# Kernel optimization log

Measured on AMD Instinct MI355X. Metric: run time of the kernel, lower is better.

## Reference

```python
import jax, jax.numpy as jnp
import numpy as np

EMB, HEADS = 1024, 16
HEAD_DIM = EMB // HEADS


def _linear(x, W, b):
    # torch nn.Linear convention: x @ W.T + b, W: [out, in]
    return jnp.einsum('bse,oe->bso', x, W) + b


def setup_inputs() -> dict:
    key = jax.random.key(0)
    ks = jax.random.split(key, 11)
    B, S = 2, 2048
    sc = 1.0 / np.sqrt(EMB)
    inp = {
        'x': jax.random.normal(ks[0], (B, S, EMB), dtype=jnp.float32),
        'y': jax.random.normal(ks[1], (B, S, EMB), dtype=jnp.float32),
        'mask': jnp.ones((B, S, S), dtype=jnp.int32),
        'Wq': jax.random.normal(ks[2], (EMB, EMB), dtype=jnp.float32) * sc,
        'bq': jax.random.normal(ks[3], (EMB,), dtype=jnp.float32) * sc,
        'Wk': jax.random.normal(ks[4], (EMB, EMB), dtype=jnp.float32) * sc,
        'bk': jax.random.normal(ks[5], (EMB,), dtype=jnp.float32) * sc,
        'Wv': jax.random.normal(ks[6], (EMB, EMB), dtype=jnp.float32) * sc,
        'bv': jax.random.normal(ks[7], (EMB,), dtype=jnp.float32) * sc,
        'Wo': jax.random.normal(ks[8], (EMB, EMB), dtype=jnp.float32) * sc,
        'bo': jax.random.normal(ks[9], (EMB,), dtype=jnp.float32) * sc,
    }
    return inp


def reference(x, y, mask, Wq, bq, Wk, bk, Wv, bv, Wo, bo):
    B, S, _ = x.shape
    q = _linear(x, Wq, bq).reshape(B, S, HEADS, HEAD_DIM).transpose(0, 2, 1, 3)
    k = _linear(y, Wk, bk).reshape(B, -1, HEADS, HEAD_DIM).transpose(0, 2, 1, 3)
    v = _linear(y, Wv, bv).reshape(B, -1, HEADS, HEAD_DIM).transpose(0, 2, 1, 3)
    # scores: [B, H, Sq, Sk]
    score = jnp.einsum('bhqd,bhkd->bhqk', q, k) / jnp.sqrt(jnp.float32(HEAD_DIM))
    # NOTE: original torch code calls score.masked_fill(...) without assignment,
    # so the mask has no effect on the computation (faithfully ignored here).
    weights = jax.nn.softmax(score, axis=-1)
    attn = jnp.einsum('bhqk,bhkd->bhqd', weights, v)
    attn = attn.transpose(0, 2, 1, 3).reshape(B, S, EMB)
    # dropout is identity in eval mode
    return _linear(attn, Wo, bo)
```

## Files before the change

kernel.cpp:

```cpp
#include <hip/hip_runtime.h>
#include <cstdint>
#include <cstddef>

#define BB 2
#define SS 2048
#define EE 1024
#define HH 16
#define DD 64

typedef __attribute__((ext_vector_type(8))) short short8;
typedef __attribute__((ext_vector_type(4))) short shortx4;
typedef __attribute__((ext_vector_type(8))) unsigned short ushort8;
typedef __attribute__((ext_vector_type(4))) unsigned short ush4;
typedef __attribute__((ext_vector_type(4))) float floatx4;

#define MFMA32(a, b, c) __builtin_amdgcn_mfma_f32_16x16x32_bf16((a), (b), (c), 0, 0, 0)
#define MFMA16(a, b, c) __builtin_amdgcn_mfma_f32_16x16x16bf16_1k((a), (b), (c), 0, 0, 0)

#define QSCALE 0.18033688011112042f

#define G2L16(g, l)                                                        \
    __builtin_amdgcn_global_load_lds(                                      \
        (const __attribute__((address_space(1))) void*)(g),                \
        (__attribute__((address_space(3))) void*)(l), 16, 0, 0)

__device__ __forceinline__ unsigned short f2bf(float f) {
    unsigned int u = __float_as_uint(f);
    u += 0x7fffu + ((u >> 16) & 1u);
    return (unsigned short)(u >> 16);
}

__device__ __forceinline__ unsigned int pkbf(float a, float b) {
    return __builtin_amdgcn_perm(__float_as_uint(b) + 0x8000u,
                                 __float_as_uint(a) + 0x8000u, 0x07060302u);
}

__global__ __launch_bounds__(256) void k_cvt(
    const float* __restrict__ x, unsigned short* __restrict__ xb,
    const float* __restrict__ y, unsigned short* __restrict__ yb,
    const float* __restrict__ w0, unsigned short* __restrict__ d0,
    const float* __restrict__ w1, unsigned short* __restrict__ d1,
    const float* __restrict__ w2, unsigned short* __restrict__ d2,
    const float* __restrict__ w3, unsigned short* __restrict__ d3)
{
    const int g = blockIdx.y;
    if (g >= 2 && blockIdx.x >= 256) return;
    const float* s = (g == 0) ? x : (g == 1) ? y : (g == 2) ? w0
                   : (g == 3) ? w1 : (g == 4) ? w2 : w3;
    unsigned short* d = (g == 0) ? xb : (g == 1) ? yb : (g == 2) ? d0
                      : (g == 3) ? d1 : (g == 4) ? d2 : d3;
    const size_t i = ((size_t)blockIdx.x * 256 + threadIdx.x) * 16;
    floatx4 f0 = *(const floatx4*)(s + i);
    floatx4 f1 = *(const floatx4*)(s + i + 4);
    floatx4 f2 = *(const floatx4*)(s + i + 8);
    floatx4 f3 = *(const floatx4*)(s + i + 12);
    ushort8 o0, o1;
#pragma unroll
    for (int j = 0; j < 4; ++j) { o0[j] = f2bf(f0[j]); o0[j + 4] = f2bf(f1[j]); }
#pragma unroll
    for (int j = 0; j < 4; ++j) { o1[j] = f2bf(f2[j]); o1[j + 4] = f2bf(f3[j]); }
    *(ushort8*)(d + i) = o0;
    *(ushort8*)(d + i + 8) = o1;
}

template <int MT, int OMODE>
__device__ __forceinline__ void gemm_body(
    const unsigned short* __restrict__ A, const unsigned short* __restrict__ W,
    const float* __restrict__ bias, void* __restrict__ Cv, float oscale,
    int m0, int n0,
    unsigned short* As0, unsigned short* As1, unsigned short* As2,
    unsigned short* Bs0, unsigned short* Bs1, unsigned short* Bs2)
{
    constexpr int K = 1024, N = 1024, LDT = 32;
    constexpr int MFR = MT / 32;
    constexpr int KEEP = (MT == 128) ? 8 : 6;
    const int t = threadIdx.x;
    const int lane = t & 63, w = t >> 6;
    const int q = lane >> 4, c = lane & 15;
    const int wm = w & 1, wn = w >> 1;
    const int lr = lane >> 2, lc = (lane & 3) * 8;

    const unsigned short* gA0 = A + (size_t)(m0 + w * (MT / 4) + lr) * K + lc;
    const unsigned short* gA1 = gA0 + 16 * K;
    const unsigned short* gB0 = W + (size_t)(n0 + w * 32 + lr) * K + lc;
    const unsigned short* gB1 = gB0 + 16 * K;
    unsigned short* lA0 = As0 + (w * (MT / 4)) * LDT;
    unsigned short* lA1 = As1 + (w * (MT / 4)) * LDT;
    unsigned short* lA2 = As2 + (w * (MT / 4)) * LDT;
    unsigned short* lB0 = Bs0 + (w * 32) * LDT;
    unsigned short* lB1 = Bs1 + (w * 32) * LDT;
    unsigned short* lB2 = Bs2 + (w * 32) * LDT;

    floatx4 acc[MFR][4] = {};

    auto compute = [&](const unsigned short* Ah, const unsigned short* Bh) {
        short8 af[MFR], bfr[4];
#pragma unroll
        for (int mi = 0; mi < MFR; ++mi)
            af[mi] = *(const short8*)
                &Ah[(wm * (MFR * 16) + mi * 16 + c) * LDT + q * 8];
#pragma unroll
        for (int ni = 0; ni < 4; ++ni)
            bfr[ni] = *(const short8*)
                &Bh[(wn * 64 + ni * 16 + c) * LDT + q * 8];
#pragma unroll
        for (int mi = 0; mi < MFR; ++mi)
#pragma unroll
            for (int ni = 0; ni < 4; ++ni)
                acc[mi][ni] = MFMA32(af[mi], bfr[ni], acc[mi][ni]);
    };

    auto stage = [&](int nk, unsigned short* lA, unsigned short* lB) {
        G2L16(gA0 + nk, lA);
        if constexpr (MT == 128) G2L16(gA1 + nk, lA + 16 * LDT);
        G2L16(gB0 + nk, lB);
        G2L16(gB1 + nk, lB + 16 * LDT);
    };

    auto phase = [&](int knext, unsigned short* lAn, unsigned short* lBn,
                     const unsigned short* Ac, const unsigned short* Bc) {
        __builtin_amdgcn_s_barrier();
        stage(knext & (K - 1), lAn, lBn);
        asm volatile("s_waitcnt vmcnt(%0)" :: "n"(KEEP) : "memory");
        __builtin_amdgcn_s_barrier();
        __builtin_amdgcn_sched_barrier(0);
        compute(Ac, Bc);
    };

    stage(0, lA0, lB0);
    stage(32, lA1, lB1);

    for (int g = 0; g < 10; ++g) {
        const int kb = g * 96;
        phase(kb +  64, lA2, lB2, As0, Bs0);
        phase(kb +  96, lA0, lB0, As1, Bs1);
        phase(kb + 128, lA1, lB1, As2, Bs2);
    }
    phase(1056, lA2, lB2, As0, Bs0);
    phase(1088, lA0, lB0, As1, Bs1);
    asm volatile("s_waitcnt vmcnt(0)" ::: "memory");

#pragma unroll
    for (int ni = 0; ni < 4; ++ni) {
        const int col = n0 + wn * 64 + ni * 16 + c;
        const float bv = bias[col];
#pragma unroll
        for (int mi = 0; mi < MFR; ++mi)
#pragma unroll
            for (int r = 0; r < 4; ++r) {
                const int row = m0 + wm * (MFR * 16) + mi * 16 + q * 4 + r;
                const float v = (acc[mi][ni][r] + bv) * oscale;
                if constexpr (OMODE == 0) {
                    ((unsigned short*)Cv)[(size_t)row * N + col] = f2bf(v);
                } else if constexpr (OMODE == 1) {
                    const int b = row >> 11, s = row & 2047;
                    ((unsigned short*)Cv)[((size_t)(b * 1024 + col)) * SS + s] = f2bf(v);
                } else {
                    ((float*)Cv)[(size_t)row * N + col] = v;
                }
            }
    }
}

__global__ __launch_bounds__(256) void k_gemm_qkv(
    const unsigned short* __restrict__ x, const unsigned short* __restrict__ y,
    const unsigned short* __restrict__ Wq, const float* __restrict__ bq,
    const unsigned short* __restrict__ Wk, const float* __restrict__ bk,
    const unsigned short* __restrict__ Wv, const float* __restrict__ bv,
    unsigned short* __restrict__ Q, unsigned short* __restrict__ Ko,
    unsigned short* __restrict__ Vt)
{
    __shared__ __align__(16) unsigned short As0[128 * 32], As1[128 * 32],
                                            As2[128 * 32];
    __shared__ __align__(16) unsigned short Bs0[128 * 32], Bs1[128 * 32],
                                            Bs2[128 * 32];
    const int m0 = blockIdx.y * 128;
    const int nt = blockIdx.x;
    const int g = nt >> 3;
    const int n0 = (nt & 7) * 128;
    if (g == 0) {
        gemm_body<128, 0>(x, Wq, bq, Q, QSCALE, m0, n0,
                          As0, As1, As2, Bs0, Bs1, Bs2);
    } else if (g == 1) {
        gemm_body<128, 0>(y, Wk, bk, Ko, 1.0f, m0, n0,
                          As0, As1, As2, Bs0, Bs1, Bs2);
    } else {
        gemm_body<128, 1>(y, Wv, bv, Vt, 1.0f, m0, n0,
                          As0, As1, As2, Bs0, Bs1, Bs2);
    }
}

__global__ __launch_bounds__(256) void k_gemm_out(
    const unsigned short* __restrict__ A, const unsigned short* __restrict__ W,
    const float* __restrict__ bias, float* __restrict__ C)
{
    __shared__ __align__(16) unsigned short As0[64 * 32], As1[64 * 32],
                                            As2[64 * 32];
    __shared__ __align__(16) unsigned short Bs0[128 * 32], Bs1[128 * 32],
                                            Bs2[128 * 32];
    gemm_body<64, 2>(A, W, bias, C, 1.0f, blockIdx.y * 64, blockIdx.x * 128,
                     As0, As1, As2, Bs0, Bs1, Bs2);
}

__global__ __launch_bounds__(512, 4) void k_attn(
    const unsigned short* __restrict__ Q, const unsigned short* __restrict__ K,
    const unsigned short* __restrict__ Vt, unsigned short* __restrict__ O)
{
    constexpr int LDK = 72;
    constexpr int TSZ = 64 * LDK + 64 * 64;
    __shared__ __align__(16) unsigned short smem[2 * 2 * TSZ];
    float* Ob = (float*)smem;

    const int bh = blockIdx.x, qt = blockIdx.y;
    const int b = bh >> 4, h = bh & 15;
    const int t = threadIdx.x, w = t >> 6;
    const int ws = w >> 2;
    const int wq = w & 3;
    const int lane = t & 63, q = lane >> 4, c = lane & 15;

    unsigned short* Sb = smem + ws * (2 * TSZ);

    short8 qb[2][2];
#pragma unroll
    for (int g = 0; g < 2; ++g) {
        const size_t qoff =
            (size_t)(b * SS + qt * 128 + wq * 32 + g * 16 + c) * EE + h * DD + q * 8;
        qb[g][0] = *(const short8*)(Q + qoff);
        qb[g][1] = *(const short8*)(Q + qoff + 32);
    }

    floatx4 o[2][4] = {};
    floatx4 lacc[2] = {};
    const shortx4 ones = {(short)0x3F80, (short)0x3F80, (short)0x3F80, (short)0x3F80};

    const int ts = t & 255;
    const int sr = ts >> 2, sp = (ts & 3) * 16;
    const int vkey = (sr & 15) << 2;
    const unsigned short* Kg =
        K + (size_t)(b * SS + ws * 1024 + sr) * EE + h * DD + sp;
    const unsigned short* Vg =
        Vt + ((size_t)bh * DD + sr) * SS + ws * 1024 + sp;

    {
        const ushort8* gk = (const ushort8*)Kg;
        ushort8 k0 = gk[0], k1 = gk[1];
        const ushort8* gv = (const ushort8*)Vg;
        ushort8 v0 = gv[0], v1 = gv[1];
        unsigned short* Ks = Sb;
        unsigned short* Vs = Sb + 64 * LDK;
        *(ushort8*)&Ks[sr * LDK + sp] = k0;
        *(ushort8*)&Ks[sr * LDK + sp + 8] = k1;
        *(ush4*)&Vs[sr * 64 + ((sp +  0) ^ vkey)] =
            __builtin_shufflevector(v0, v0, 0, 1, 2, 3);
        *(ush4*)&Vs[sr * 64 + ((sp +  4) ^ vkey)] =
            __builtin_shufflevector(v0, v0, 4, 5, 6, 7);
        *(ush4*)&Vs[sr * 64 + ((sp +  8) ^ vkey)] =
            __builtin_shufflevector(v1, v1, 0, 1, 2, 3);
        *(ush4*)&Vs[sr * 64 + ((sp + 12) ^ vkey)] =
            __builtin_shufflevector(v1, v1, 4, 5, 6, 7);
    }

#pragma unroll 2
    for (int it = 0; it < 16; ++it) {
        const unsigned short* Ks = Sb + (it & 1) * TSZ;
        const unsigned short* Vs = Ks + 64 * LDK;
        __syncthreads();

        const int nit = (it + 1) & 15;
        ushort8 pk0, pk1, pv0, pv1;
        {
            const ushort8* gk = (const ushort8*)(Kg + (size_t)nit * 64 * EE);
            pk0 = gk[0]; pk1 = gk[1];
            const ushort8* gv = (const ushort8*)(Vg + nit * 64);
            pv0 = gv[0]; pv1 = gv[1];
        }

#pragma unroll
        for (int tt = 0; tt < 4; ++tt) {
            const short8 ka0 = *(const short8*)&Ks[(tt * 16 + c) * LDK + q * 8];
            const short8 ka1 = *(const short8*)&Ks[(tt * 16 + c) * LDK + 32 + q * 8];
            shortx4 pa[2];
#pragma unroll
            for (int g = 0; g < 2; ++g) {
                floatx4 s = {0.f, 0.f, 0.f, 0.f};
                s = MFMA32(ka0, qb[g][0], s);
                s = MFMA32(ka1, qb[g][1], s);
                union { unsigned int u[2]; shortx4 v; } pk;
                pk.u[0] = pkbf(__builtin_amdgcn_exp2f(s[0]),
                               __builtin_amdgcn_exp2f(s[1]));
                pk.u[1] = pkbf(__builtin_amdgcn_exp2f(s[2]),
                               __builtin_amdgcn_exp2f(s[3]));
                pa[g] = pk.v;
            }
#pragma unroll
            for (int nd = 0; nd < 4; ++nd) {
                const shortx4 vb = *(const shortx4*)
                    &Vs[(nd * 16 + c) * 64 + (((tt * 4 + q) ^ c) << 2)];
                o[0][nd] = MFMA16(pa[0], vb, o[0][nd]);
                o[1][nd] = MFMA16(pa[1], vb, o[1][nd]);
            }
            lacc[0] = MFMA16(pa[0], ones, lacc[0]);
            lacc[1] = MFMA16(pa[1], ones, lacc[1]);
        }

        {
            unsigned short* Kn = Sb + ((it + 1) & 1) * TSZ;
            unsigned short* Vn = Kn + 64 * LDK;
            *(ushort8*)&Kn[sr * LDK + sp] = pk0;
            *(ushort8*)&Kn[sr * LDK + sp + 8] = pk1;
            *(ush4*)&Vn[sr * 64 + ((sp +  0) ^ vkey)] =
                __builtin_shufflevector(pv0, pv0, 0, 1, 2, 3);
            *(ush4*)&Vn[sr * 64 + ((sp +  4) ^ vkey)] =
                __builtin_shufflevector(pv0, pv0, 4, 5, 6, 7);
            *(ush4*)&Vn[sr * 64 + ((sp +  8) ^ vkey)] =
                __builtin_shufflevector(pv1, pv1, 0, 1, 2, 3);
            *(ush4*)&Vn[sr * 64 + ((sp + 12) ^ vkey)] =
                __builtin_shufflevector(pv1, pv1, 4, 5, 6, 7);
        }
    }

    __syncthreads();
    if (ws == 1) {
#pragma unroll
        for (int g = 0; g < 2; ++g) {
#pragma unroll
            for (int nd = 0; nd < 4; ++nd)
#pragma unroll
                for (int r = 0; r < 4; ++r)
                    Ob[(wq * 32 + g * 16 + q * 4 + r) * 66 + nd * 16 + c] =
                        o[g][nd][r];
            if (c == 0) {
#pragma unroll
                for (int r = 0; r < 4; ++r)
                    Ob[(wq * 32 + g * 16 + q * 4 + r) * 66 + 64] = lacc[g][r];
            }
        }
    }
    __syncthreads();
    if (ws == 0) {
#pragma unroll
        for (int g = 0; g < 2; ++g) {
            float linv[4];
#pragma unroll
            for (int r = 0; r < 4; ++r) {
                const int rr = wq * 32 + g * 16 + q * 4 + r;
#pragma unroll
                for (int nd = 0; nd < 4; ++nd)
                    o[g][nd][r] += Ob[rr * 66 + nd * 16 + c];
                linv[r] = __builtin_amdgcn_rcpf(lacc[g][r] + Ob[rr * 66 + 64]);
            }
            const int orow = b * SS + qt * 128 + wq * 32 + g * 16;
#pragma unroll
            for (int nd = 0; nd < 4; ++nd)
#pragma unroll
                for (int r = 0; r < 4; ++r)
                    O[(size_t)(orow + q * 4 + r) * EE + h * DD + nd * 16 + c] =
                        f2bf(o[g][nd][r] * linv[r]);
        }
    }
}

extern "C" void kernel_launch(void* const* d_in, const int* in_sizes, int n_in,
                              void* d_out, int out_size, void* d_ws, size_t ws_size,
                              hipStream_t stream)
{
    const float* x  = (const float*)d_in[0];
    const float* y  = (const float*)d_in[1];
    const float* Wq = (const float*)d_in[3];
    const float* bq = (const float*)d_in[4];
    const float* Wk = (const float*)d_in[5];
    const float* bk = (const float*)d_in[6];
    const float* Wv = (const float*)d_in[7];
    const float* bv = (const float*)d_in[8];
    const float* Wo = (const float*)d_in[9];
    const float* bo = (const float*)d_in[10];
    float* out = (float*)d_out;

    char* ws = (char*)d_ws;
    const size_t SZ = (size_t)BB * SS * EE * sizeof(unsigned short);
    const size_t WZ = (size_t)EE * EE * sizeof(unsigned short);
    unsigned short* xb  = (unsigned short*)(ws);
    unsigned short* yb  = (unsigned short*)(ws + SZ);
    unsigned short* Wqb = (unsigned short*)(ws + 2 * SZ);
    unsigned short* Wkb = (unsigned short*)(ws + 2 * SZ + WZ);
    unsigned short* Wvb = (unsigned short*)(ws + 2 * SZ + 2 * WZ);
    unsigned short* Wob = (unsigned short*)(ws + 2 * SZ + 3 * WZ);
    unsigned short* Qw  = (unsigned short*)(ws + 2 * SZ + 4 * WZ);
    unsigned short* Kw  = (unsigned short*)(ws + 3 * SZ + 4 * WZ);
    unsigned short* Vtw = (unsigned short*)(ws + 4 * SZ + 4 * WZ);
    unsigned short* Aw  = (unsigned short*)(ws + 5 * SZ + 4 * WZ);
    (void)ws_size; (void)in_sizes; (void)n_in; (void)out_size;

    k_cvt<<<dim3(1024, 6), 256, 0, stream>>>(x, xb, y, yb, Wq, Wqb, Wk, Wkb,
                                             Wv, Wvb, Wo, Wob);
    k_gemm_qkv<<<dim3(24, 32), 256, 0, stream>>>(xb, yb, Wqb, bq, Wkb, bk, Wvb, bv,
                                                 Qw, Kw, Vtw);
    k_attn<<<dim3(32, 16), 512, 0, stream>>>(Qw, Kw, Vtw, Aw);
    k_gemm_out<<<dim3(8, 64), 256, 0, stream>>>(Aw, Wob, bo, out);
}
```

Baseline: 226.1 us.

## Prefetch K/V two tiles ahead in attention and enlarge out-projection tiles

The attention loop now holds K/V loads for two future tiles in registers and issues each global load two iterations before use, which is meant to hide global memory latency better. It also swaps __syncthreads for a raw s_barrier plus sched_barrier fences and explicit lgkmcnt waits. Separately, the output projection GEMM moves from 64x128 to 128x128 tiles with half as many blocks. The costs are higher register pressure in attention and fewer, larger workgroups in the output GEMM.

New measurement: 229.9 us. Within noise of the previous version (+1.7%).

```diff
diff --git a/kernel.cpp b/kernel.cpp
--- a/kernel.cpp
+++ b/kernel.cpp
@@ -194,12 +194,12 @@
     const unsigned short* __restrict__ A, const unsigned short* __restrict__ W,
     const float* __restrict__ bias, float* __restrict__ C)
 {
-    __shared__ __align__(16) unsigned short As0[64 * 32], As1[64 * 32],
-                                            As2[64 * 32];
+    __shared__ __align__(16) unsigned short As0[128 * 32], As1[128 * 32],
+                                            As2[128 * 32];
     __shared__ __align__(16) unsigned short Bs0[128 * 32], Bs1[128 * 32],
                                             Bs2[128 * 32];
-    gemm_body<64, 2>(A, W, bias, C, 1.0f, blockIdx.y * 64, blockIdx.x * 128,
-                     As0, As1, As2, Bs0, Bs1, Bs2);
+    gemm_body<128, 2>(A, W, bias, C, 1.0f, blockIdx.y * 128, blockIdx.x * 128,
+                      As0, As1, As2, Bs0, Bs1, Bs2);
 }
 
 __global__ __launch_bounds__(512, 4) void k_attn(
@@ -241,13 +241,8 @@
     const unsigned short* Vg =
         Vt + ((size_t)bh * DD + sr) * SS + ws * 1024 + sp;
 
-    {
-        const ushort8* gk = (const ushort8*)Kg;
-        ushort8 k0 = gk[0], k1 = gk[1];
-        const ushort8* gv = (const ushort8*)Vg;
-        ushort8 v0 = gv[0], v1 = gv[1];
-        unsigned short* Ks = Sb;
-        unsigned short* Vs = Sb + 64 * LDK;
+    auto put = [&](unsigned short* Ks, unsigned short* Vs,
+                   ushort8 k0, ushort8 k1, ushort8 v0, ushort8 v1) {
         *(ushort8*)&Ks[sr * LDK + sp] = k0;
         *(ushort8*)&Ks[sr * LDK + sp + 8] = k1;
         *(ush4*)&Vs[sr * 64 + ((sp +  0) ^ vkey)] =
@@ -258,21 +253,35 @@
             __builtin_shufflevector(v1, v1, 0, 1, 2, 3);
         *(ush4*)&Vs[sr * 64 + ((sp + 12) ^ vkey)] =
             __builtin_shufflevector(v1, v1, 4, 5, 6, 7);
+    };
+
+    ushort8 rk[2][2], rv[2][2];
+    {
+        const ushort8* gk0 = (const ushort8*)Kg;
+        rk[0][0] = gk0[0]; rk[0][1] = gk0[1];
+        const ushort8* gv0 = (const ushort8*)Vg;
+        rv[0][0] = gv0[0]; rv[0][1] = gv0[1];
+        const ushort8* gk1 = (const ushort8*)(Kg + (size_t)64 * EE);
+        rk[1][0] = gk1[0]; rk[1][1] = gk1[1];
+        const ushort8* gv1 = (const ushort8*)(Vg + 64);
+        rv[1][0] = gv1[0]; rv[1][1] = gv1[1];
+        put(Sb, Sb + 64 * LDK, rk[0][0], rk[0][1], rv[0][0], rv[0][1]);
+        asm volatile("s_waitcnt lgkmcnt(0)" ::: "memory");
     }
 
 #pragma unroll 2
     for (int it = 0; it < 16; ++it) {
         const unsigned short* Ks = Sb + (it & 1) * TSZ;
         const unsigned short* Vs = Ks + 64 * LDK;
-        __syncthreads();
-
-        const int nit = (it + 1) & 15;
-        ushort8 pk0, pk1, pv0, pv1;
+        __builtin_amdgcn_s_barrier();
+        __builtin_amdgcn_sched_barrier(0);
+
         {
+            const int nit = (it + 2) & 15;
             const ushort8* gk = (const ushort8*)(Kg + (size_t)nit * 64 * EE);
-            pk0 = gk[0]; pk1 = gk[1];
+            rk[it & 1][0] = gk[0]; rk[it & 1][1] = gk[1];
             const ushort8* gv = (const ushort8*)(Vg + nit * 64);
-            pv0 = gv[0]; pv1 = gv[1];
+            rv[it & 1][0] = gv[0]; rv[it & 1][1] = gv[1];
         }
 
 #pragma unroll
@@ -303,20 +312,14 @@
             lacc[1] = MFMA16(pa[1], ones, lacc[1]);
         }
 
+        __builtin_amdgcn_sched_barrier(0);
         {
             unsigned short* Kn = Sb + ((it + 1) & 1) * TSZ;
             unsigned short* Vn = Kn + 64 * LDK;
-            *(ushort8*)&Kn[sr * LDK + sp] = pk0;
-            *(ushort8*)&Kn[sr * LDK + sp + 8] = pk1;
-            *(ush4*)&Vn[sr * 64 + ((sp +  0) ^ vkey)] =
-                __builtin_shufflevector(pv0, pv0, 0, 1, 2, 3);
-            *(ush4*)&Vn[sr * 64 + ((sp +  4) ^ vkey)] =
-                __builtin_shufflevector(pv0, pv0, 4, 5, 6, 7);
-            *(ush4*)&Vn[sr * 64 + ((sp +  8) ^ vkey)] =
-                __builtin_shufflevector(pv1, pv1, 0, 1, 2, 3);
-            *(ush4*)&Vn[sr * 64 + ((sp + 12) ^ vkey)] =
-                __builtin_shufflevector(pv1, pv1, 4, 5, 6, 7);
+            put(Kn, Vn, rk[(it + 1) & 1][0], rk[(it + 1) & 1][1],
+                rv[(it + 1) & 1][0], rv[(it + 1) & 1][1]);
         }
+        asm volatile("s_waitcnt lgkmcnt(0)" ::: "memory");
     }
 
     __syncthreads();
@@ -396,5 +399,5 @@
     k_gemm_qkv<<<dim3(24, 32), 256, 0, stream>>>(xb, yb, Wqb, bq, Wkb, bk, Wvb, bv,
                                                  Qw, Kw, Vtw);
     k_attn<<<dim3(32, 16), 512, 0, stream>>>(Qw, Kw, Vtw, Aw);
-    k_gemm_out<<<dim3(8, 64), 256, 0, stream>>>(Aw, Wob, bo, out);
-}
+    k_gemm_out<<<dim3(8, 32), 256, 0, stream>>>(Aw, Wob, bo, out);
+}
```
